# Kernel optimization log

Measured on AMD Instinct MI355X. Metric: run time of the kernel, lower is better.

Reference implementation:

```python
import jax, jax.numpy as jnp
import numpy as np

B, C, T = 16, 128, 4096
Q, K = 8, 1024


def setup_inputs() -> dict:
    key = jax.random.key(0)
    k1, k2 = jax.random.split(key)
    latents = jax.random.normal(k1, (B, C, T), dtype=jnp.float32)
    embeddings = jax.random.normal(k2, (Q, K, C), dtype=jnp.float32)
    return {"latents": latents, "embeddings": embeddings}


def reference(latents, embeddings):
    # latents: [B, C, T]; embeddings: [Q, K, C]
    b, c, t = latents.shape
    q = embeddings.shape[0]
    flat = latents.transpose(0, 2, 1).reshape(-1, c)  # [N, C], N = B*T

    def stage(carry, emb):
        residual, qsum, closs = carry
        # squared euclidean distances [N, K] via expansion identity
        d = ((residual * residual).sum(axis=1, keepdims=True)
             - 2.0 * residual @ emb.T
             + (emb * emb).sum(axis=1))
        idx = jnp.argmin(d, axis=1)          # [N]
        quant = emb[idx]                     # [N, C] gather
        closs = closs + jnp.mean((residual - jax.lax.stop_gradient(quant)) ** 2)
        return (residual - quant, qsum + quant, closs), idx

    init = (flat, jnp.zeros_like(flat), jnp.zeros((), dtype=flat.dtype))
    (_, qsum, closs), codes = jax.lax.scan(stage, init, embeddings)

    quantized = qsum.reshape(b, t, c).transpose(0, 2, 1)       # [B, C, T]
    codes = codes.reshape(q, b, t).transpose(1, 0, 2)          # [B, Q, T]
    commitment_loss = closs / q
    codebook_loss = jnp.zeros((), dtype=latents.dtype)
    return quantized, codes, commitment_loss, codebook_loss
```

## Files before the change

kernel.cpp:

```cpp
#include <hip/hip_runtime.h>

#define Bq 16
#define Cc 128
#define Tt 4096
#define Qq 8
#define Kk 1024
#define Nn (Bq*Tt)

#define ROWS 128
#define NTC  256
#define KCH  32
#define NTILES (Kk/NTC)
#define KCHUNKS (Cc/KCH)

typedef float f32x4 __attribute__((ext_vector_type(4)));
typedef float f32x8 __attribute__((ext_vector_type(8)));
typedef int   i32x8 __attribute__((ext_vector_type(8)));

static __device__ __forceinline__ f32x8 splat8(float x) {
    f32x8 v = {x, x, x, x, x, x, x, x};
    return v;
}

__global__ __launch_bounds__(256) void ee_kernel(const float* __restrict__ emb,
                                                 float* __restrict__ ee,
                                                 double* __restrict__ closs) {
    int i = blockIdx.x * 256 + threadIdx.x;
    if (i == 0) *closs = 0.0;
    if (i < Qq * Kk) {
        const float* e = emb + (size_t)i * Cc;
        float s0 = 0.f, s1 = 0.f, s2 = 0.f, s3 = 0.f;
#pragma unroll
        for (int c = 0; c < Cc; c += 4) {
            s0 = fmaf(e[c],     e[c],     s0);
            s1 = fmaf(e[c + 1], e[c + 1], s1);
            s2 = fmaf(e[c + 2], e[c + 2], s2);
            s3 = fmaf(e[c + 3], e[c + 3], s3);
        }
        ee[i] = (s0 + s1) + (s2 + s3);
    }
}

__global__ __launch_bounds__(512, 2) void vq_kernel(
    const float* __restrict__ latents,
    const float* __restrict__ emb,
    const float* __restrict__ ee,
    float* __restrict__ quantized,
    float* __restrict__ codes,
    double* __restrict__ closs)
{
    extern __shared__ float smem[];
    float* r_lds  = smem;
    float* B_lds  = smem + Cc * ROWS;
    float* rrp    = B_lds + KCH * NTC;
    float* rr_lds = rrp + 4 * ROWS;
    int*   win    = (int*)(rr_lds + ROWS);

    const int t   = threadIdx.x;
    const int tx  = t & 31;
    const int ty  = t >> 5;
    const int un  = t & 127;
    const int ukg = t >> 7;

    const int rowbase = blockIdx.x * ROWS;
    const int bb  = rowbase >> 12;
    const int tt0 = rowbase & (Tt - 1);

    {
        const float* lb = latents + (size_t)bb * Cc * Tt + tt0 + un;
        float part = 0.f;
#pragma unroll
        for (int j = 0; j < KCH; ++j) {
            int k = ukg * KCH + j;
            float v = lb[(size_t)k * Tt];
            r_lds[k * ROWS + un] = v;
            part = fmaf(v, v, part);
        }
        rrp[ukg * ROWS + un] = part;
    }
    __syncthreads();
    if (t < ROWS)
        rr_lds[t] = (rrp[t] + rrp[ROWS + t]) + (rrp[2 * ROWS + t] + rrp[3 * ROWS + t]);
    __syncthreads();

    for (int q = 0; q < Qq; ++q) {
        const float* eq = emb + (size_t)q * Kk * Cc;

        f32x8 best_ = splat8(3.4e38f);
        i32x8 bk_   = {0, 0, 0, 0, 0, 0, 0, 0};
        f32x8 rr8   = *(const f32x8*)&rr_lds[ty * 8];

        for (int nt = 0; nt < NTILES; ++nt) {
            f32x8 acc0 = splat8(0.f), acc1 = splat8(0.f), acc2 = splat8(0.f), acc3 = splat8(0.f);
            f32x8 acc4 = splat8(0.f), acc5 = splat8(0.f), acc6 = splat8(0.f), acc7 = splat8(0.f);

            for (int kc = 0; kc < KCHUNKS; ++kc) {
                __syncthreads();
                {
                    const int cl = t >> 1;
                    const int hk = (t & 1) * 16;
                    const float* src = eq + (size_t)(nt * NTC + cl) * Cc + kc * KCH + hk;
#pragma unroll
                    for (int j = 0; j < 4; ++j) {
                        f32x4 v = *(const f32x4*)(src + j * 4);
#pragma unroll
                        for (int i2 = 0; i2 < 4; ++i2)
                            B_lds[(hk + j * 4 + i2) * NTC + cl] = v[i2];
                    }
                }
                __syncthreads();

#pragma unroll 8
                for (int kk = 0; kk < KCH; ++kk) {
                    f32x8 a_ = *(const f32x8*)&r_lds[(kc * KCH + kk) * ROWS + ty * 8];
                    f32x8 b_ = *(const f32x8*)&B_lds[kk * NTC + tx * 8];
                    acc0 = __builtin_elementwise_fma(splat8(a_[0]), b_, acc0);
                    acc1 = __builtin_elementwise_fma(splat8(a_[1]), b_, acc1);
                    acc2 = __builtin_elementwise_fma(splat8(a_[2]), b_, acc2);
                    acc3 = __builtin_elementwise_fma(splat8(a_[3]), b_, acc3);
                    acc4 = __builtin_elementwise_fma(splat8(a_[4]), b_, acc4);
                    acc5 = __builtin_elementwise_fma(splat8(a_[5]), b_, acc5);
                    acc6 = __builtin_elementwise_fma(splat8(a_[6]), b_, acc6);
                    acc7 = __builtin_elementwise_fma(splat8(a_[7]), b_, acc7);
                }
            }

            f32x8 ee_ = *(const f32x8*)(ee + q * Kk + nt * NTC + tx * 8);
            const int kbase = nt * NTC + tx * 8;
#define FOLD_ROW(I_) {                                                        \
            f32x8 dv = __builtin_elementwise_fma(splat8(-2.0f), acc##I_,      \
                                                 splat8(rr8[I_])) + ee_;      \
            _Pragma("unroll")                                                 \
            for (int c = 0; c < 8; ++c) {                                     \
                float d = dv[c];                                              \
                bool lt = d < best_[I_];                                      \
                best_[I_] = lt ? d : best_[I_];                               \
                bk_[I_]   = lt ? (kbase + c) : bk_[I_];                       \
            } }
            FOLD_ROW(0) FOLD_ROW(1) FOLD_ROW(2) FOLD_ROW(3)
            FOLD_ROW(4) FOLD_ROW(5) FOLD_ROW(6) FOLD_ROW(7)
#undef FOLD_ROW
        }

#pragma unroll
        for (int m = 1; m < 32; m <<= 1) {
#pragma unroll
            for (int i = 0; i < 8; ++i) {
                float od = __shfl_xor(best_[i], m);
                int   ok = __shfl_xor(bk_[i], m);
                bool rep = (od < best_[i]) || (od == best_[i] && ok < bk_[i]);
                best_[i] = rep ? od : best_[i];
                bk_[i]   = rep ? ok : bk_[i];
            }
        }
        if (tx == 0) {
#pragma unroll
            for (int i = 0; i < 8; ++i) {
                int row = ty * 8 + i;
                win[row] = bk_[i];
                codes[((size_t)bb * Qq + q) * Tt + tt0 + row] = (float)bk_[i];
            }
        }
        __syncthreads();

        {
            const float* er = eq + (size_t)win[un] * Cc + ukg * KCH;
            float part = 0.f;
#pragma unroll
            for (int j = 0; j < 8; ++j) {
                f32x4 ev = *(const f32x4*)(er + j * 4);
#pragma unroll
                for (int i2 = 0; i2 < 4; ++i2) {
                    int k = ukg * KCH + j * 4 + i2;
                    float rv = r_lds[k * ROWS + un] - ev[i2];
                    r_lds[k * ROWS + un] = rv;
                    part = fmaf(rv, rv, part);
                }
            }
            rrp[ukg * ROWS + un] = part;
        }
        __syncthreads();
        if (t < ROWS)
            rr_lds[t] = (rrp[t] + rrp[ROWS + t]) + (rrp[2 * ROWS + t] + rrp[3 * ROWS + t]);
        __syncthreads();
        if (t < 64) {
            double s = (double)rr_lds[t] + (double)rr_lds[t + 64];
#pragma unroll
            for (int off = 32; off; off >>= 1)
                s += __shfl_down(s, off);
            if (t == 0) atomicAdd(closs, s);
        }
    }

    {
        const float* lb = latents + (size_t)bb * Cc * Tt + tt0 + un;
        float* qb = quantized + (size_t)bb * Cc * Tt + tt0 + un;
#pragma unroll
        for (int j = 0; j < KCH; ++j) {
            int k = ukg * KCH + j;
            qb[(size_t)k * Tt] = lb[(size_t)k * Tt] - r_lds[k * ROWS + un];
        }
    }
}

__global__ void fin_kernel(const double* __restrict__ closs, float* __restrict__ loss_out) {
    loss_out[0] = (float)(*closs / (double)((size_t)Nn * Cc * Qq));
    loss_out[1] = 0.0f;
}

extern "C" void kernel_launch(void* const* d_in, const int* in_sizes, int n_in,
                              void* d_out, int out_size, void* d_ws, size_t ws_size,
                              hipStream_t stream) {
    const float* latents = (const float*)d_in[0];
    const float* emb     = (const float*)d_in[1];
    float* out       = (float*)d_out;
    float* quantized = out;
    float* codes     = out + (size_t)Bq * Cc * Tt;
    float* loss      = codes + (size_t)Bq * Qq * Tt;
    double* closs    = (double*)d_ws;
    float*  ee       = (float*)((char*)d_ws + 64);

    const size_t smem = (size_t)(Cc * ROWS + KCH * NTC + 4 * ROWS + ROWS) * sizeof(float)
                      + ROWS * sizeof(int);
    (void)hipFuncSetAttribute((const void*)vq_kernel,
                              hipFuncAttributeMaxDynamicSharedMemorySize, (int)smem);

    ee_kernel<<<(Qq * Kk + 255) / 256, 256, 0, stream>>>(emb, ee, closs);
    vq_kernel<<<Nn / ROWS, 512, smem, stream>>>(latents, emb, ee, quantized, codes, closs);
    fin_kernel<<<1, 1, 0, stream>>>(closs, loss);
}
```

Before: 1.807 ms.

## Double-buffer codebook tiles in LDS with register prefetch and conflict-free column mapping

The codebook-tile staging is now double-buffered in LDS. The next 32x256 chunk is loaded into registers while the current chunk's FMA loop runs, then written into the alternate buffer, which leaves one barrier per chunk instead of two. The tile and chunk loops are flattened into a single loop that resets the accumulators at each tile start. Each thread now reads codebook columns as two 4-wide groups (tx*4 and tx*4+128) rather than 8 contiguous columns, meant to reduce LDS bank conflicts, and the code index used in the argmin fold is remapped to match. The cost is an extra 32 KB of LDS and more live registers for the prefetch.

Measured after the change: 1.759 ms. 2.6% less time.

```diff
diff --git a/kernel.cpp b/kernel.cpp
--- a/kernel.cpp
+++ b/kernel.cpp
@@ -12,6 +12,7 @@
 #define KCH  32
 #define NTILES (Kk/NTC)
 #define KCHUNKS (Cc/KCH)
+#define NCHUNK (NTILES*KCHUNKS)
 
 typedef float f32x4 __attribute__((ext_vector_type(4)));
 typedef float f32x8 __attribute__((ext_vector_type(8)));
@@ -52,7 +53,7 @@
     extern __shared__ float smem[];
     float* r_lds  = smem;
     float* B_lds  = smem + Cc * ROWS;
-    float* rrp    = B_lds + KCH * NTC;
+    float* rrp    = B_lds + 2 * KCH * NTC;
     float* rr_lds = rrp + 4 * ROWS;
     int*   win    = (int*)(rr_lds + ROWS);
 
@@ -61,6 +62,8 @@
     const int ty  = t >> 5;
     const int un  = t & 127;
     const int ukg = t >> 7;
+    const int cl  = t >> 1;
+    const int hk  = (t & 1) * 16;
 
     const int rowbase = blockIdx.x * ROWS;
     const int bb  = rowbase >> 12;
@@ -90,56 +93,95 @@
         i32x8 bk_   = {0, 0, 0, 0, 0, 0, 0, 0};
         f32x8 rr8   = *(const f32x8*)&rr_lds[ty * 8];
 
-        for (int nt = 0; nt < NTILES; ++nt) {
-            f32x8 acc0 = splat8(0.f), acc1 = splat8(0.f), acc2 = splat8(0.f), acc3 = splat8(0.f);
-            f32x8 acc4 = splat8(0.f), acc5 = splat8(0.f), acc6 = splat8(0.f), acc7 = splat8(0.f);
-
-            for (int kc = 0; kc < KCHUNKS; ++kc) {
-                __syncthreads();
-                {
-                    const int cl = t >> 1;
-                    const int hk = (t & 1) * 16;
-                    const float* src = eq + (size_t)(nt * NTC + cl) * Cc + kc * KCH + hk;
-#pragma unroll
-                    for (int j = 0; j < 4; ++j) {
-                        f32x4 v = *(const f32x4*)(src + j * 4);
-#pragma unroll
-                        for (int i2 = 0; i2 < 4; ++i2)
-                            B_lds[(hk + j * 4 + i2) * NTC + cl] = v[i2];
-                    }
-                }
-                __syncthreads();
-
+        {
+            const float* src = eq + (size_t)cl * Cc + hk;
+            f32x4 pf0 = *(const f32x4*)(src);
+            f32x4 pf1 = *(const f32x4*)(src + 4);
+            f32x4 pf2 = *(const f32x4*)(src + 8);
+            f32x4 pf3 = *(const f32x4*)(src + 12);
+#pragma unroll
+            for (int i2 = 0; i2 < 4; ++i2) B_lds[(hk +      i2) * NTC + cl] = pf0[i2];
+#pragma unroll
+            for (int i2 = 0; i2 < 4; ++i2) B_lds[(hk +  4 + i2) * NTC + cl] = pf1[i2];
+#pragma unroll
+            for (int i2 = 0; i2 < 4; ++i2) B_lds[(hk +  8 + i2) * NTC + cl] = pf2[i2];
+#pragma unroll
+            for (int i2 = 0; i2 < 4; ++i2) B_lds[(hk + 12 + i2) * NTC + cl] = pf3[i2];
+        }
+        __syncthreads();
+
+        f32x8 acc0, acc1, acc2, acc3, acc4, acc5, acc6, acc7;
+
+        for (int id = 0; id < NCHUNK; ++id) {
+            const int nt  = id >> 2;
+            const int kc  = id & 3;
+            const int cur = id & 1;
+            if (kc == 0) {
+                acc0 = splat8(0.f); acc1 = splat8(0.f); acc2 = splat8(0.f); acc3 = splat8(0.f);
+                acc4 = splat8(0.f); acc5 = splat8(0.f); acc6 = splat8(0.f); acc7 = splat8(0.f);
+            }
+
+            f32x4 pf0, pf1, pf2, pf3;
+            if (id < NCHUNK - 1) {
+                const int nid = id + 1;
+                const float* src = eq + (size_t)(((nid >> 2) * NTC) + cl) * Cc
+                                 + (nid & 3) * KCH + hk;
+                pf0 = *(const f32x4*)(src);
+                pf1 = *(const f32x4*)(src + 4);
+                pf2 = *(const f32x4*)(src + 8);
+                pf3 = *(const f32x4*)(src + 12);
+            }
+
+            const float* Bb = B_lds + cur * (KCH * NTC);
 #pragma unroll 8
-                for (int kk = 0; kk < KCH; ++kk) {
-                    f32x8 a_ = *(const f32x8*)&r_lds[(kc * KCH + kk) * ROWS + ty * 8];
-                    f32x8 b_ = *(const f32x8*)&B_lds[kk * NTC + tx * 8];
-                    acc0 = __builtin_elementwise_fma(splat8(a_[0]), b_, acc0);
-                    acc1 = __builtin_elementwise_fma(splat8(a_[1]), b_, acc1);
-                    acc2 = __builtin_elementwise_fma(splat8(a_[2]), b_, acc2);
-                    acc3 = __builtin_elementwise_fma(splat8(a_[3]), b_, acc3);
-                    acc4 = __builtin_elementwise_fma(splat8(a_[4]), b_, acc4);
-                    acc5 = __builtin_elementwise_fma(splat8(a_[5]), b_, acc5);
-                    acc6 = __builtin_elementwise_fma(splat8(a_[6]), b_, acc6);
-                    acc7 = __builtin_elementwise_fma(splat8(a_[7]), b_, acc7);
-                }
-            }
-
-            f32x8 ee_ = *(const f32x8*)(ee + q * Kk + nt * NTC + tx * 8);
-            const int kbase = nt * NTC + tx * 8;
+            for (int kk = 0; kk < KCH; ++kk) {
+                f32x8 a_  = *(const f32x8*)&r_lds[(kc * KCH + kk) * ROWS + ty * 8];
+                f32x4 blo = *(const f32x4*)&Bb[kk * NTC + tx * 4];
+                f32x4 bhi = *(const f32x4*)&Bb[kk * NTC + 128 + tx * 4];
+                f32x8 b_  = __builtin_shufflevector(blo, bhi, 0, 1, 2, 3, 4, 5, 6, 7);
+                acc0 = __builtin_elementwise_fma(splat8(a_[0]), b_, acc0);
+                acc1 = __builtin_elementwise_fma(splat8(a_[1]), b_, acc1);
+                acc2 = __builtin_elementwise_fma(splat8(a_[2]), b_, acc2);
+                acc3 = __builtin_elementwise_fma(splat8(a_[3]), b_, acc3);
+                acc4 = __builtin_elementwise_fma(splat8(a_[4]), b_, acc4);
+                acc5 = __builtin_elementwise_fma(splat8(a_[5]), b_, acc5);
+                acc6 = __builtin_elementwise_fma(splat8(a_[6]), b_, acc6);
+                acc7 = __builtin_elementwise_fma(splat8(a_[7]), b_, acc7);
+            }
+
+            if (id < NCHUNK - 1) {
+                float* Bn = B_lds + (cur ^ 1) * (KCH * NTC);
+#pragma unroll
+                for (int i2 = 0; i2 < 4; ++i2) Bn[(hk +      i2) * NTC + cl] = pf0[i2];
+#pragma unroll
+                for (int i2 = 0; i2 < 4; ++i2) Bn[(hk +  4 + i2) * NTC + cl] = pf1[i2];
+#pragma unroll
+                for (int i2 = 0; i2 < 4; ++i2) Bn[(hk +  8 + i2) * NTC + cl] = pf2[i2];
+#pragma unroll
+                for (int i2 = 0; i2 < 4; ++i2) Bn[(hk + 12 + i2) * NTC + cl] = pf3[i2];
+            }
+            __syncthreads();
+
+            if (kc == 3) {
+                const int kb = nt * NTC + tx * 4;
+                f32x4 eelo = *(const f32x4*)(ee + q * Kk + kb);
+                f32x4 eehi = *(const f32x4*)(ee + q * Kk + kb + 128);
+                f32x8 ee_  = __builtin_shufflevector(eelo, eehi, 0, 1, 2, 3, 4, 5, 6, 7);
 #define FOLD_ROW(I_) {                                                        \
-            f32x8 dv = __builtin_elementwise_fma(splat8(-2.0f), acc##I_,      \
-                                                 splat8(rr8[I_])) + ee_;      \
-            _Pragma("unroll")                                                 \
-            for (int c = 0; c < 8; ++c) {                                     \
-                float d = dv[c];                                              \
-                bool lt = d < best_[I_];                                      \
-                best_[I_] = lt ? d : best_[I_];                               \
-                bk_[I_]   = lt ? (kbase + c) : bk_[I_];                       \
-            } }
-            FOLD_ROW(0) FOLD_ROW(1) FOLD_ROW(2) FOLD_ROW(3)
-            FOLD_ROW(4) FOLD_ROW(5) FOLD_ROW(6) FOLD_ROW(7)
+                f32x8 dv = __builtin_elementwise_fma(splat8(-2.0f), acc##I_,  \
+                                                     splat8(rr8[I_])) + ee_;  \
+                _Pragma("unroll")                                             \
+                for (int c = 0; c < 8; ++c) {                                 \
+                    float d = dv[c];                                          \
+                    int code = kb + (c < 4 ? c : c + 124);                    \
+                    bool lt = d < best_[I_];                                  \
+                    best_[I_] = lt ? d : best_[I_];                           \
+                    bk_[I_]   = lt ? code : bk_[I_];                          \
+                } }
+                FOLD_ROW(0) FOLD_ROW(1) FOLD_ROW(2) FOLD_ROW(3)
+                FOLD_ROW(4) FOLD_ROW(5) FOLD_ROW(6) FOLD_ROW(7)
 #undef FOLD_ROW
+            }
         }
 
 #pragma unroll
@@ -220,7 +262,7 @@
     double* closs    = (double*)d_ws;
     float*  ee       = (float*)((char*)d_ws + 64);
 
-    const size_t smem = (size_t)(Cc * ROWS + KCH * NTC + 4 * ROWS + ROWS) * sizeof(float)
+    const size_t smem = (size_t)(Cc * ROWS + 2 * KCH * NTC + 4 * ROWS + ROWS) * sizeof(float)
                       + ROWS * sizeof(int);
     (void)hipFuncSetAttribute((const void*)vq_kernel,
                               hipFuncAttributeMaxDynamicSharedMemorySize, (int)smem);
```
